# Kernel optimization log

Hardware: AMD Instinct MI355X
Metric: run time of the kernel (lower is better)

Reference implementation:

```python
import jax, jax.numpy as jnp
import numpy as np
import math

S, H, NH, HD = 2048, 1280, 16, 80
WIN = 64
NW = S // WIN
I = 3420
OUT = 3584
L = 8
FULL_IDX = (3, 7)
MERGE = 4  # spatial_merge_size**2
EPS = 1e-6


def setup_inputs() -> dict:
    key = jax.random.key(0)
    ks = jax.random.split(key, 16)
    w = lambda k, s: jax.random.normal(k, s, jnp.float32) * 0.02
    # rotary tables: half-dim freqs duplicated, as in Qwen2.5-VL vision rotary
    inv_freq = 1.0 / (10000.0 ** (np.arange(0, HD // 2, dtype=np.float32) / (HD // 2)))
    freqs = np.outer(np.arange(S, dtype=np.float32), inv_freq)  # [S, HD/2]
    emb = np.concatenate([freqs, freqs], axis=-1)               # [S, HD]
    return {
        "hidden_states": jax.random.normal(ks[0], (S, H), jnp.float32),
        "full_attn_masks": jnp.ones((1, 1, S, S), jnp.float32),
        "window_attn_masks": jnp.ones((NW, 1, WIN, WIN), jnp.float32),
        "cos": jnp.asarray(np.cos(emb)),
        "sin": jnp.asarray(np.sin(emb)),
        "qkv_w": w(ks[1], (L, 3 * H, H)),
        "qkv_b": w(ks[2], (L, 3 * H)),
        "proj_w": w(ks[3], (L, H, H)),
        "proj_b": w(ks[4], (L, H)),
        "norm1_w": jnp.ones((L, H), jnp.float32),
        "norm2_w": jnp.ones((L, H), jnp.float32),
        "gate_w": w(ks[5], (L, I, H)),
        "gate_b": w(ks[6], (L, I)),
        "up_w": w(ks[7], (L, I, H)),
        "up_b": w(ks[8], (L, I)),
        "down_w": w(ks[9], (L, H, I)),
        "down_b": w(ks[10], (L, H)),
        "ln_q_w": jnp.ones((H,), jnp.float32),
        "m0_w": w(ks[11], (H * MERGE, H * MERGE)),
        "m0_b": w(ks[12], (H * MERGE,)),
        "m2_w": w(ks[13], (OUT, H * MERGE)),
        "m2_b": w(ks[14], (OUT,)),
    }


def rmsnorm(x, w):
    v = jnp.mean(jnp.square(x.astype(jnp.float32)), axis=-1, keepdims=True)
    return (x * jax.lax.rsqrt(v + EPS)) * w


def rotate_half(x):
    x1, x2 = jnp.split(x, 2, axis=-1)
    return jnp.concatenate([-x2, x1], axis=-1)


def apply_rope(q, k, cos, sin):
    return q * cos + rotate_half(q) * sin, k * cos + rotate_half(k) * sin


def attn_full(x, mask, cos, sin, qkv_w, qkv_b, proj_w, proj_b):
    # x: [S, H]; mask: [1, 1, S, S] (additive)
    qkv = (x @ qkv_w.T + qkv_b).reshape(S, 3, NH, HD)
    q, k, v = [t[:, i].transpose(1, 0, 2) for i, t in [(0, qkv), (1, qkv), (2, qkv)]]  # [NH, S, HD]
    q, k = apply_rope(q, k, cos, sin)  # cos/sin [S, HD] broadcast over heads
    aw = jnp.einsum('hsd,htd->hst', q, k) / math.sqrt(HD) + mask[0]
    aw = jax.nn.softmax(aw.astype(jnp.float32), axis=-1)
    o = jnp.einsum('hst,htd->hsd', aw, v).transpose(1, 0, 2).reshape(S, NH * HD)
    return o @ proj_w.T + proj_b


def attn_window(x, mask, cos, sin, qkv_w, qkv_b, proj_w, proj_b):
    xw = x.reshape(NW, WIN, H)
    qkv = (xw @ qkv_w.T + qkv_b).reshape(NW, WIN, 3, NH, HD).transpose(2, 0, 3, 1, 4)
    q, k, v = qkv[0], qkv[1], qkv[2]
    cw = cos.reshape(NW, 1, WIN, HD)
    sw = sin.reshape(NW, 1, WIN, HD)
    q, k = apply_rope(q, k, cw, sw)
    aw = jnp.einsum('whsd,whtd->whst', q, k) / math.sqrt(HD) + mask
    aw = jax.nn.softmax(aw.astype(jnp.float32), axis=-1)
    o = jnp.einsum('whst,whtd->whsd', aw, v).transpose(0, 2, 1, 3).reshape(S, NH * HD)
    return o @ proj_w.T + proj_b


def reference(hidden_states, full_attn_masks, window_attn_masks, cos, sin,
              qkv_w, qkv_b, proj_w, proj_b, norm1_w, norm2_w,
              gate_w, gate_b, up_w, up_b, down_w, down_b,
              ln_q_w, m0_w, m0_b, m2_w, m2_b):
    NEG = jnp.finfo(jnp.float32).min
    fm = (1.0 - full_attn_masks) * NEG
    wm = (1.0 - window_attn_masks) * NEG
    x = hidden_states
    for i in range(L):
        h = rmsnorm(x, norm1_w[i])
        if i in FULL_IDX:
            a = attn_full(h, fm, cos, sin, qkv_w[i], qkv_b[i], proj_w[i], proj_b[i])
        else:
            a = attn_window(h, wm, cos, sin, qkv_w[i], qkv_b[i], proj_w[i], proj_b[i])
        x = x + a
        h = rmsnorm(x, norm2_w[i])
        mlp = (jax.nn.silu(h @ gate_w[i].T + gate_b[i]) * (h @ up_w[i].T + up_b[i])) @ down_w[i].T + down_b[i]
        x = x + mlp
    # patch merger: RMSNorm -> merge 4 tokens -> Linear-GELU-Linear
    h = rmsnorm(x, ln_q_w).reshape(-1, H * MERGE)  # [S/4, 5120]
    h = jax.nn.gelu(h @ m0_w.T + m0_b, approximate=False)
    return h @ m2_w.T + m2_b  # [S/4, OUT]
```

## Files before the change

kernel.cpp:

```cpp
#include <hip/hip_runtime.h>
#include <hip/hip_bf16.h>
#include <math.h>

#define S_LEN 2048
#define HID   1280
#define NHEADS 16
#define HDIM  80
#define HDP   96
#define LAYERS 8
#define IDIM  3420
#define IDIMP 3456
#define MERGED 5120
#define OUTD  3584
#define NCH   4
#define CHLEN 512

typedef __attribute__((ext_vector_type(8))) short short8;
typedef __attribute__((ext_vector_type(4))) float f32x4;
typedef unsigned int u32;
typedef __attribute__((address_space(1))) const u32* gptr_t;
typedef __attribute__((address_space(3))) u32* lptr_t;

__device__ inline unsigned short f2b(float f){
  __hip_bfloat16 b = __float2bfloat16(f);
  return __builtin_bit_cast(unsigned short, b);
}
__device__ inline float b2f(unsigned short u){
  return __bfloat162float(__builtin_bit_cast(__hip_bfloat16, u));
}
__device__ inline unsigned pk2(float lo, float hi){
  return (unsigned)f2b(lo) | ((unsigned)f2b(hi) << 16);
}

__global__ __launch_bounds__(256) void convert_kernel(
    const float* __restrict__ src, unsigned short* __restrict__ dst,
    int N, int K, int Np, int Kp)
{
  int kg = Kp >> 3;
  size_t total = (size_t)Np * kg;
  for (size_t i = (size_t)blockIdx.x * 256 + threadIdx.x; i < total;
       i += (size_t)gridDim.x * 256){
    int k8 = (int)(i % kg);
    int n  = (int)(i / kg);
    int k0 = k8 * 8;
    u32 out[4];
    if (n < N && k0 + 8 <= K){
      const float* s = src + (size_t)n * K + k0;
      float4 f0 = *(const float4*)s;
      float4 f1 = *(const float4*)(s + 4);
      out[0] = pk2(f0.x, f0.y); out[1] = pk2(f0.z, f0.w);
      out[2] = pk2(f1.x, f1.y); out[3] = pk2(f1.z, f1.w);
    } else {
      #pragma unroll
      for (int j = 0; j < 4; ++j){
        int ka = k0 + 2 * j;
        float lo = (n < N && ka     < K) ? src[(size_t)n * K + ka]     : 0.f;
        float hi = (n < N && ka + 1 < K) ? src[(size_t)n * K + ka + 1] : 0.f;
        out[j] = pk2(lo, hi);
      }
    }
    *(uint4*)(dst + i * 8) = make_uint4(out[0], out[1], out[2], out[3]);
  }
}

__global__ __launch_bounds__(256) void concat_bias_kernel(
    const float* __restrict__ g, const float* __restrict__ u, float* __restrict__ o)
{
  int n = blockIdx.x * 256 + threadIdx.x;
  if (n >= 2 * IDIMP) return;
  if (n < IDIMP) o[n] = (n < IDIM) ? g[n] : 0.f;
  else { int m2 = n - IDIMP; o[n] = (m2 < IDIM) ? u[m2] : 0.f; }
}

__global__ __launch_bounds__(256) void rmsnorm_kernel(
    const float* __restrict__ x, const float* __restrict__ w,
    unsigned short* __restrict__ out, int H)
{
  int s = blockIdx.x;
  const float* row = x + (size_t)s * H;
  float ss = 0.f;
  for (int c = threadIdx.x; c < H; c += 256){ float v = row[c]; ss += v * v; }
  #pragma unroll
  for (int off = 32; off >= 1; off >>= 1) ss += __shfl_xor(ss, off, 64);
  __shared__ float red[4];
  if ((threadIdx.x & 63) == 0) red[threadIdx.x >> 6] = ss;
  __syncthreads();
  ss = red[0] + red[1] + red[2] + red[3];
  float rs = rsqrtf(ss / H + 1e-6f);
  unsigned short* orow = out + (size_t)s * H;
  for (int c = threadIdx.x; c < H; c += 256) orow[c] = f2b(row[c] * rs * w[c]);
}

template<int EPI, int BM>
__global__ __launch_bounds__(256) void gemm_kernel(
    const unsigned short* __restrict__ A, int lda,
    const unsigned short* __restrict__ B, int ldb,
    const float* __restrict__ bias, int Nact,
    void* __restrict__ Cv, int ldc,
    const float* __restrict__ res,
    int K)
{
  constexpr int MI = BM / 32;
  __shared__ __align__(16) unsigned short As[2][BM * 32];
  __shared__ __align__(16) unsigned short Bs[2][4096];
  const int tid  = threadIdx.x;
  const int lane = tid & 63;
  const int wave = tid >> 6;
  const int wm = wave >> 1, wn = wave & 1;
  const int m0 = blockIdx.y * BM, n0 = blockIdx.x * 128;
  const int l16 = lane & 15, lh = lane >> 4;
  const int lrow = lane >> 2;
  const int lcol = lane & 3;
  f32x4 acc[MI][4] = {};

  auto stage = [&](int bufi, int k0){
    #pragma unroll
    for (int j = 0; j < BM / 64; ++j){
      int chunk = wave * (BM / 64) + j;
      int row  = chunk * 16 + lrow;
      int slot = lcol ^ ((row >> 1) & 3);
      const unsigned short* srcA = A + (size_t)(m0 + row) * lda + k0 + slot * 8;
      __builtin_amdgcn_global_load_lds((gptr_t)srcA, (lptr_t)&As[bufi][chunk * 512], 16, 0, 0);
    }
    #pragma unroll
    for (int j = 0; j < 2; ++j){
      int chunk = wave * 2 + j;
      int row  = chunk * 16 + lrow;
      int slot = lcol ^ ((row >> 1) & 3);
      const unsigned short* srcB = B + (size_t)(n0 + row) * ldb + k0 + slot * 8;
      __builtin_amdgcn_global_load_lds((gptr_t)srcB, (lptr_t)&Bs[bufi][chunk * 512], 16, 0, 0);
    }
  };

  const int nt = K >> 5;
  stage(0, 0);
  __syncthreads();
  int buf = 0;
  for (int t = 0; t < nt; ++t){
    if (t + 1 < nt) stage(buf ^ 1, (t + 1) << 5);
    short8 af[MI], bfr[4];
    #pragma unroll
    for (int mi = 0; mi < MI; ++mi){
      int r = wm * (BM / 2) + mi * 16 + l16;
      int sl = lh ^ ((r >> 1) & 3);
      af[mi] = *(const short8*)&As[buf][r * 32 + sl * 8];
    }
    #pragma unroll
    for (int ni = 0; ni < 4; ++ni){
      int r = wn * 64 + ni * 16 + l16;
      int sl = lh ^ ((r >> 1) & 3);
      bfr[ni] = *(const short8*)&Bs[buf][r * 32 + sl * 8];
    }
    #pragma unroll
    for (int mi = 0; mi < MI; ++mi)
      #pragma unroll
      for (int ni = 0; ni < 4; ++ni)
        acc[mi][ni] = __builtin_amdgcn_mfma_f32_16x16x32_bf16(af[mi], bfr[ni], acc[mi][ni], 0, 0, 0);
    __syncthreads();
    buf ^= 1;
  }

  #pragma unroll
  for (int mi = 0; mi < MI; ++mi){
    int row = m0 + wm * (BM / 2) + mi * 16 + lh * 4;
    #pragma unroll
    for (int ni = 0; ni < 4; ++ni){
      int gn = n0 + wn * 64 + ni * 16 + l16;
      float bv = (gn < Nact) ? bias[gn] : 0.f;
      #pragma unroll
      for (int r2 = 0; r2 < 4; ++r2){
        float v = acc[mi][ni][r2] + bv;
        size_t offc = (size_t)(row + r2) * ldc + gn;
        if (EPI == 0)      ((float*)Cv)[offc] = v;
        else if (EPI == 1) ((float*)Cv)[offc] = res[offc] + v;
        else if (EPI == 2) ((unsigned short*)Cv)[offc] = f2b(0.5f * v * (1.0f + erff(v * 0.70710678118f)));
        else               ((unsigned short*)Cv)[offc] = f2b(v);
      }
    }
  }
}

__global__ __launch_bounds__(256) void rope_split_kernel(
    const unsigned short* __restrict__ qkv, const float* __restrict__ cosT,
    const float* __restrict__ sinT,
    unsigned short* __restrict__ qo, unsigned short* __restrict__ ko,
    unsigned short* __restrict__ vt)
{
  int s = blockIdx.x;
  const unsigned short* row = qkv + (size_t)s * 3840;
  #pragma unroll
  for (int it = 0; it < 5; ++it){
    int idx = it * 256 + threadIdx.x;
    int h = idx / 80, d = idx % 80;
    float qv = b2f(row[h * 80 + d]);
    float kv = b2f(row[1280 + h * 80 + d]);
    float vv = b2f(row[2560 + h * 80 + d]);
    float c  = cosT[s * 80 + d], sn = sinT[s * 80 + d];
    float qr = (d < 40) ? -b2f(row[h * 80 + d + 40])        : b2f(row[h * 80 + d - 40]);
    float kr = (d < 40) ? -b2f(row[1280 + h * 80 + d + 40]) : b2f(row[1280 + h * 80 + d - 40]);
    size_t qkoff = ((size_t)h * S_LEN + s) * HDP + d;
    qo[qkoff] = f2b(qv * c + qr * sn);
    ko[qkoff] = f2b(kv * c + kr * sn);
    vt[((size_t)h * HDIM + d) * S_LEN + s] = f2b(vv);
  }
  int h2 = threadIdx.x >> 4, d2 = 80 + (threadIdx.x & 15);
  size_t poff = ((size_t)h2 * S_LEN + s) * HDP + d2;
  qo[poff] = 0; ko[poff] = 0;
}

template<int PART>
__global__ __launch_bounds__(256) void flash_kernel(
    const unsigned short* __restrict__ q, const unsigned short* __restrict__ k,
    const unsigned short* __restrict__ vt, unsigned short* __restrict__ out,
    float* __restrict__ opart, float* __restrict__ mlpart)
{
  __shared__ __align__(16) unsigned short P[4][16][80];
  const int lane = threadIdx.x & 63;
  const int w = threadIdx.x >> 6;
  const int h = blockIdx.y;
  const int q0 = blockIdx.x * 64;
  const int ch = PART ? blockIdx.z : 0;
  const int qr = q0 + w * 16;
  const int l16 = lane & 15, lh = lane >> 4;
  const unsigned short* qh = q + (size_t)h * S_LEN * HDP;
  const unsigned short* kh = k + (size_t)h * S_LEN * HDP;
  const unsigned short* vh = vt + (size_t)h * HDIM * S_LEN;

  short8 qa[3];
  #pragma unroll
  for (int kc = 0; kc < 3; ++kc)
    qa[kc] = *(const short8*)(qh + (size_t)(qr + l16) * HDP + kc * 32 + lh * 8);

  float m_[4] = {-1e30f, -1e30f, -1e30f, -1e30f};
  float l_[4] = {0.f, 0.f, 0.f, 0.f};
  f32x4 o_[5] = {};
  const int kvb = PART ? ch * CHLEN : q0;
  const int kve = PART ? ch * CHLEN + CHLEN : q0 + 64;

  for (int kv0 = kvb; kv0 < kve; kv0 += 64){
    f32x4 sc[4] = {};
    #pragma unroll
    for (int nf = 0; nf < 4; ++nf){
      const unsigned short* krow = kh + (size_t)(kv0 + nf * 16 + l16) * HDP + lh * 8;
      #pragma unroll
      for (int kc = 0; kc < 3; ++kc){
        short8 bfr = *(const short8*)(krow + kc * 32);
        sc[nf] = __builtin_amdgcn_mfma_f32_16x16x32_bf16(qa[kc], bfr, sc[nf], 0, 0, 0);
      }
    }
    const float scale = 0.11180339887498949f;
    #pragma unroll
    for (int r = 0; r < 4; ++r){
      float t = fmaxf(fmaxf(sc[0][r], sc[1][r]), fmaxf(sc[2][r], sc[3][r])) * scale;
      t = fmaxf(t, __shfl_xor(t, 1, 64));
      t = fmaxf(t, __shfl_xor(t, 2, 64));
      t = fmaxf(t, __shfl_xor(t, 4, 64));
      t = fmaxf(t, __shfl_xor(t, 8, 64));
      float mnew = fmaxf(m_[r], t);
      float corr = __expf(m_[r] - mnew);
      float rs = 0.f;
      #pragma unroll
      for (int nf = 0; nf < 4; ++nf){
        float p = __expf(sc[nf][r] * scale - mnew);
        sc[nf][r] = p;
        rs += p;
      }
      rs += __shfl_xor(rs, 1, 64);
      rs += __shfl_xor(rs, 2, 64);
      rs += __shfl_xor(rs, 4, 64);
      rs += __shfl_xor(rs, 8, 64);
      l_[r] = l_[r] * corr + rs;
      m_[r] = mnew;
      #pragma unroll
      for (int of = 0; of < 5; ++of) o_[of][r] *= corr;
    }
    #pragma unroll
    for (int nf = 0; nf < 4; ++nf)
      #pragma unroll
      for (int r = 0; r < 4; ++r)
        P[w][lh * 4 + r][nf * 16 + l16] = f2b(sc[nf][r]);
    #pragma unroll
    for (int kc2 = 0; kc2 < 2; ++kc2){
      short8 pa = *(const short8*)&P[w][l16][kc2 * 32 + lh * 8];
      #pragma unroll
      for (int of = 0; of < 5; ++of){
        short8 bv = *(const short8*)(vh + (size_t)(of * 16 + l16) * S_LEN + kv0 + kc2 * 32 + lh * 8);
        o_[of] = __builtin_amdgcn_mfma_f32_16x16x32_bf16(pa, bv, o_[of], 0, 0, 0);
      }
    }
  }
  if (PART){
    const size_t base = ((size_t)(ch * NHEADS + h) * S_LEN);
    #pragma unroll
    for (int of = 0; of < 5; ++of)
      #pragma unroll
      for (int r = 0; r < 4; ++r)
        opart[(base + qr + lh * 4 + r) * HDIM + of * 16 + l16] = o_[of][r];
    if (l16 == 0){
      #pragma unroll
      for (int r = 0; r < 4; ++r){
        mlpart[(base + qr + lh * 4 + r) * 2 + 0] = m_[r];
        mlpart[(base + qr + lh * 4 + r) * 2 + 1] = l_[r];
      }
    }
  } else {
    #pragma unroll
    for (int of = 0; of < 5; ++of)
      #pragma unroll
      for (int r = 0; r < 4; ++r){
        size_t off = (size_t)(qr + lh * 4 + r) * HID + h * HDIM + of * 16 + l16;
        out[off] = f2b(o_[of][r] / l_[r]);
      }
  }
}

__global__ __launch_bounds__(256) void flash_reduce_kernel(
    const float* __restrict__ opart, const float* __restrict__ mlpart,
    unsigned short* __restrict__ out)
{
  int idx = blockIdx.x * 256 + threadIdx.x;
  if (idx >= NHEADS * S_LEN * HDIM) return;
  int d = idx % HDIM; int rem = idx / HDIM;
  int qi = rem % S_LEN; int h = rem / S_LEN;
  float mv[NCH];
  float M = -1e30f;
  #pragma unroll
  for (int c = 0; c < NCH; ++c){
    mv[c] = mlpart[((size_t)(c * NHEADS + h) * S_LEN + qi) * 2];
    M = fmaxf(M, mv[c]);
  }
  float L = 0.f, O = 0.f;
  #pragma unroll
  for (int c = 0; c < NCH; ++c){
    float wgt = __expf(mv[c] - M);
    L += wgt * mlpart[((size_t)(c * NHEADS + h) * S_LEN + qi) * 2 + 1];
    O += wgt * opart[((size_t)(c * NHEADS + h) * S_LEN + qi) * HDIM + d];
  }
  out[(size_t)qi * HID + h * HDIM + d] = f2b(O / L);
}

__global__ __launch_bounds__(256) void silu_mul_kernel(
    const float* __restrict__ gu, unsigned short* __restrict__ out)
{
  size_t i = ((size_t)blockIdx.x * 256 + threadIdx.x) * 4;
  if (i >= (size_t)S_LEN * IDIMP) return;
  int row = (int)(i / IDIMP), col = (int)(i % IDIMP);
  float4 gv = *(const float4*)(gu + (size_t)row * (2 * IDIMP) + col);
  float4 uv = *(const float4*)(gu + (size_t)row * (2 * IDIMP) + IDIMP + col);
  float r0 = gv.x / (1.f + __expf(-gv.x)) * uv.x;
  float r1 = gv.y / (1.f + __expf(-gv.y)) * uv.y;
  float r2 = gv.z / (1.f + __expf(-gv.z)) * uv.z;
  float r3 = gv.w / (1.f + __expf(-gv.w)) * uv.w;
  uint2 o;
  o.x = pk2(r0, r1); o.y = pk2(r2, r3);
  *(uint2*)(out + i) = o;
}

static inline int cgrid(size_t total){
  size_t b = (total + 255) / 256;
  return (int)(b < 4096 ? b : 4096);
}

extern "C" void kernel_launch(void* const* d_in, const int* in_sizes, int n_in,
                              void* d_out, int out_size, void* d_ws, size_t ws_size,
                              hipStream_t stream)
{
  const float* hidden = (const float*)d_in[0];
  const float* cosT   = (const float*)d_in[3];
  const float* sinT   = (const float*)d_in[4];
  const float* qkv_w  = (const float*)d_in[5];
  const float* qkv_b  = (const float*)d_in[6];
  const float* proj_w = (const float*)d_in[7];
  const float* proj_b = (const float*)d_in[8];
  const float* norm1_w= (const float*)d_in[9];
  const float* norm2_w= (const float*)d_in[10];
  const float* gate_w = (const float*)d_in[11];
  const float* gate_b = (const float*)d_in[12];
  const float* up_w   = (const float*)d_in[13];
  const float* up_b   = (const float*)d_in[14];
  const float* down_w = (const float*)d_in[15];
  const float* down_b = (const float*)d_in[16];
  const float* ln_q_w = (const float*)d_in[17];
  const float* m0_w   = (const float*)d_in[18];
  const float* m0_b   = (const float*)d_in[19];
  const float* m2_w   = (const float*)d_in[20];
  const float* m2_b   = (const float*)d_in[21];

  char* ws = (char*)d_ws;
  size_t off = 0;
  auto carve = [&](size_t bytes)->char*{
    char* p = ws + off; off += (bytes + 255) & ~(size_t)255; return p;
  };
  float*          x    = (float*)         carve((size_t)S_LEN * HID * 4);
  unsigned short* hbuf = (unsigned short*)carve((size_t)S_LEN * HID * 2);
  unsigned short* qkvb = (unsigned short*)carve((size_t)S_LEN * 3840 * 2);
  unsigned short* qp   = (unsigned short*)carve((size_t)NHEADS * S_LEN * HDP * 2);
  unsigned short* kp   = (unsigned short*)carve((size_t)NHEADS * S_LEN * HDP * 2);
  unsigned short* vtb  = (unsigned short*)carve((size_t)NHEADS * HDIM * S_LEN * 2);
  unsigned short* ao   = (unsigned short*)carve((size_t)S_LEN * HID * 2);
  float*          gbuf = (float*)         carve((size_t)S_LEN * 2 * IDIMP * 4);
  unsigned short* mlp  = (unsigned short*)carve((size_t)S_LEN * IDIMP * 2);
  unsigned short* mg   = (unsigned short*)carve((size_t)512 * MERGED * 2);
  float*          opart= (float*)         carve((size_t)NCH * NHEADS * S_LEN * HDIM * 4);
  float*          mlpt = (float*)         carve((size_t)NCH * NHEADS * S_LEN * 2 * 4);
  float*          cbias= (float*)         carve((size_t)2 * IDIMP * 4);
  unsigned short* wbig = (unsigned short*)carve((size_t)45000000 * 2);
  unsigned short* wqkv = wbig;
  unsigned short* wproj= wbig +  4915200;
  unsigned short* wgate= wproj + 1638400;
  unsigned short* wup  = wgate + (size_t)IDIMP * HID;
  unsigned short* wdown= wup   + (size_t)IDIMP * HID;
  unsigned short* wm0  = wbig;
  unsigned short* wm2  = wbig + (size_t)MERGED * MERGED;
  (void)ws_size; (void)in_sizes; (void)n_in; (void)out_size;

  hipMemcpyAsync(x, hidden, (size_t)S_LEN * HID * 4, hipMemcpyDeviceToDevice, stream);

  for (int i = 0; i < LAYERS; ++i){
    convert_kernel<<<cgrid((size_t)3840*HID/8), 256, 0, stream>>>(
        qkv_w + (size_t)i*3840*HID, wqkv, 3840, HID, 3840, HID);
    convert_kernel<<<cgrid((size_t)HID*HID/8), 256, 0, stream>>>(
        proj_w + (size_t)i*HID*HID, wproj, HID, HID, HID, HID);
    convert_kernel<<<cgrid((size_t)IDIMP*HID/8), 256, 0, stream>>>(
        gate_w + (size_t)i*IDIM*HID, wgate, IDIM, HID, IDIMP, HID);
    convert_kernel<<<cgrid((size_t)IDIMP*HID/8), 256, 0, stream>>>(
        up_w + (size_t)i*IDIM*HID, wup, IDIM, HID, IDIMP, HID);
    convert_kernel<<<cgrid((size_t)HID*IDIMP/8), 256, 0, stream>>>(
        down_w + (size_t)i*HID*IDIM, wdown, HID, IDIM, HID, IDIMP);
    concat_bias_kernel<<<27, 256, 0, stream>>>(
        gate_b + (size_t)i*IDIM, up_b + (size_t)i*IDIM, cbias);

    rmsnorm_kernel<<<S_LEN, 256, 0, stream>>>(x, norm1_w + (size_t)i * HID, hbuf, HID);
    gemm_kernel<3,128><<<dim3(30, 16), 256, 0, stream>>>(
        hbuf, HID, wqkv, HID, qkv_b + (size_t)i * 3840, 3840,
        qkvb, 3840, nullptr, HID);
    rope_split_kernel<<<S_LEN, 256, 0, stream>>>(qkvb, cosT, sinT, qp, kp, vtb);
    if (i == 3 || i == 7){
      flash_kernel<1><<<dim3(32, 16, NCH), 256, 0, stream>>>(qp, kp, vtb, nullptr, opart, mlpt);
      flash_reduce_kernel<<<(NHEADS * S_LEN * HDIM + 255) / 256, 256, 0, stream>>>(opart, mlpt, ao);
    } else {
      flash_kernel<0><<<dim3(32, 16), 256, 0, stream>>>(qp, kp, vtb, ao, nullptr, nullptr);
    }
    gemm_kernel<1,64><<<dim3(10, 32), 256, 0, stream>>>(
        ao, HID, wproj, HID, proj_b + (size_t)i * HID, HID,
        x, HID, x, HID);
    rmsnorm_kernel<<<S_LEN, 256, 0, stream>>>(x, norm2_w + (size_t)i * HID, hbuf, HID);
    gemm_kernel<0,128><<<dim3(54, 16), 256, 0, stream>>>(
        hbuf, HID, wgate, HID, cbias, 2 * IDIMP,
        gbuf, 2 * IDIMP, nullptr, HID);
    silu_mul_kernel<<<(int)(((size_t)S_LEN * IDIMP / 4 + 255) / 256), 256, 0, stream>>>(gbuf, mlp);
    gemm_kernel<1,64><<<dim3(10, 32), 256, 0, stream>>>(
        mlp, IDIMP, wdown, IDIMP, down_b + (size_t)i * HID, HID,
        x, HID, x, IDIMP);
  }
  convert_kernel<<<cgrid((size_t)MERGED*MERGED/8), 256, 0, stream>>>(
      m0_w, wm0, MERGED, MERGED, MERGED, MERGED);
  convert_kernel<<<cgrid((size_t)OUTD*MERGED/8), 256, 0, stream>>>(
      m2_w, wm2, OUTD, MERGED, OUTD, MERGED);
  rmsnorm_kernel<<<S_LEN, 256, 0, stream>>>(x, ln_q_w, hbuf, HID);
  gemm_kernel<2,64><<<dim3(40, 8), 256, 0, stream>>>(
      hbuf, MERGED, wm0, MERGED, m0_b, MERGED, mg, MERGED, nullptr, MERGED);
  gemm_kernel<0,64><<<dim3(28, 8), 256, 0, stream>>>(
      mg, MERGED, wm2, MERGED, m2_b, OUTD, d_out, OUTD, nullptr, MERGED);
}
```

Before: 2.687 ms.

## Rewrite flash attention with 32x32 MFMA, register-resident P, and lazy rescaling

Flash attention now computes S^T with 32x32x16 bf16 MFMA tiles, 32 query rows per wave and 128 per block. The probability tile stays in registers, with a cross-half lane shuffle, instead of round-tripping through LDS. Online-softmax rescaling is skipped unless the running max grows by more than a threshold. The V layout is padded to 96 rows, partial outputs are stored d-major, and the reduce kernel is restructured to normalise per row and stage output through LDS for wider stores. This cuts shuffle reductions, LDS traffic and output write overhead, at the cost of fewer blocks and higher register pressure.

```diff
diff --git a/kernel.cpp b/kernel.cpp
--- a/kernel.cpp
+++ b/kernel.cpp
@@ -7,6 +7,7 @@
 #define NHEADS 16
 #define HDIM  80
 #define HDP   96
+#define VROWS 96
 #define LAYERS 8
 #define IDIM  3420
 #define IDIMP 3456
@@ -17,7 +18,9 @@
 
 typedef __attribute__((ext_vector_type(8))) short short8;
 typedef __attribute__((ext_vector_type(4))) float f32x4;
+typedef __attribute__((ext_vector_type(16))) float f32x16;
 typedef unsigned int u32;
+typedef __attribute__((ext_vector_type(4))) u32 u32x4;
 typedef __attribute__((address_space(1))) const u32* gptr_t;
 typedef __attribute__((address_space(3))) u32* lptr_t;
 
@@ -201,7 +204,7 @@
     size_t qkoff = ((size_t)h * S_LEN + s) * HDP + d;
     qo[qkoff] = f2b(qv * c + qr * sn);
     ko[qkoff] = f2b(kv * c + kr * sn);
-    vt[((size_t)h * HDIM + d) * S_LEN + s] = f2b(vv);
+    vt[((size_t)h * VROWS + d) * S_LEN + s] = f2b(vv);
   }
   int h2 = threadIdx.x >> 4, d2 = 80 + (threadIdx.x & 15);
   size_t poff = ((size_t)h2 * S_LEN + s) * HDP + d2;
@@ -214,103 +217,116 @@
     const unsigned short* __restrict__ vt, unsigned short* __restrict__ out,
     float* __restrict__ opart, float* __restrict__ mlpart)
 {
-  __shared__ __align__(16) unsigned short P[4][16][80];
+  __shared__ unsigned short ot[4][32][88];
   const int lane = threadIdx.x & 63;
   const int w = threadIdx.x >> 6;
   const int h = blockIdx.y;
-  const int q0 = blockIdx.x * 64;
+  const int l31 = lane & 31, lh1 = lane >> 5;
+  const int qr = blockIdx.x * 128 + w * 32;
   const int ch = PART ? blockIdx.z : 0;
-  const int qr = q0 + w * 16;
-  const int l16 = lane & 15, lh = lane >> 4;
   const unsigned short* qh = q + (size_t)h * S_LEN * HDP;
   const unsigned short* kh = k + (size_t)h * S_LEN * HDP;
-  const unsigned short* vh = vt + (size_t)h * HDIM * S_LEN;
-
-  short8 qa[3];
-  #pragma unroll
-  for (int kc = 0; kc < 3; ++kc)
-    qa[kc] = *(const short8*)(qh + (size_t)(qr + l16) * HDP + kc * 32 + lh * 8);
-
-  float m_[4] = {-1e30f, -1e30f, -1e30f, -1e30f};
-  float l_[4] = {0.f, 0.f, 0.f, 0.f};
-  f32x4 o_[5] = {};
-  const int kvb = PART ? ch * CHLEN : q0;
-  const int kve = PART ? ch * CHLEN + CHLEN : q0 + 64;
-
-  for (int kv0 = kvb; kv0 < kve; kv0 += 64){
-    f32x4 sc[4] = {};
-    #pragma unroll
-    for (int nf = 0; nf < 4; ++nf){
-      const unsigned short* krow = kh + (size_t)(kv0 + nf * 16 + l16) * HDP + lh * 8;
+  const unsigned short* vh = vt + (size_t)h * VROWS * S_LEN;
+
+  short8 qa[5];
+  #pragma unroll
+  for (int kc = 0; kc < 5; ++kc)
+    qa[kc] = *(const short8*)(qh + (size_t)(qr + l31) * HDP + kc * 16 + lh1 * 8);
+
+  float m_ = -1e30f, l_ = 0.f;
+  f32x16 o0 = {}, o1 = {}, o2 = {};
+  const int kvb = PART ? ch * CHLEN : (qr & ~63);
+  const int kve = PART ? ch * CHLEN + CHLEN : (qr & ~63) + 64;
+  const float scale = 0.11180339887498949f;
+
+  for (int kvt = kvb; kvt < kve; kvt += 32){
+    f32x16 sc = {};
+    __builtin_amdgcn_s_setprio(1);
+    #pragma unroll
+    for (int kc = 0; kc < 5; ++kc){
+      short8 kf = *(const short8*)(kh + (size_t)(kvt + l31) * HDP + kc * 16 + lh1 * 8);
+      sc = __builtin_amdgcn_mfma_f32_32x32x16_bf16(kf, qa[kc], sc, 0, 0, 0);
+    }
+    __builtin_amdgcn_s_setprio(0);
+    float t = sc[0];
+    #pragma unroll
+    for (int i = 1; i < 16; ++i) t = fmaxf(t, sc[i]);
+    t = fmaxf(t, __shfl_xor(t, 32)) * scale;
+    if (!__all(t <= m_ + 8.f)){
+      float mnew = fmaxf(m_, t);
+      float corr = __expf(m_ - mnew);
+      l_ *= corr;
       #pragma unroll
-      for (int kc = 0; kc < 3; ++kc){
-        short8 bfr = *(const short8*)(krow + kc * 32);
-        sc[nf] = __builtin_amdgcn_mfma_f32_16x16x32_bf16(qa[kc], bfr, sc[nf], 0, 0, 0);
-      }
-    }
-    const float scale = 0.11180339887498949f;
-    #pragma unroll
-    for (int r = 0; r < 4; ++r){
-      float t = fmaxf(fmaxf(sc[0][r], sc[1][r]), fmaxf(sc[2][r], sc[3][r])) * scale;
-      t = fmaxf(t, __shfl_xor(t, 1, 64));
-      t = fmaxf(t, __shfl_xor(t, 2, 64));
-      t = fmaxf(t, __shfl_xor(t, 4, 64));
-      t = fmaxf(t, __shfl_xor(t, 8, 64));
-      float mnew = fmaxf(m_[r], t);
-      float corr = __expf(m_[r] - mnew);
-      float rs = 0.f;
-      #pragma unroll
-      for (int nf = 0; nf < 4; ++nf){
-        float p = __expf(sc[nf][r] * scale - mnew);
-        sc[nf][r] = p;
-        rs += p;
-      }
-      rs += __shfl_xor(rs, 1, 64);
-      rs += __shfl_xor(rs, 2, 64);
-      rs += __shfl_xor(rs, 4, 64);
-      rs += __shfl_xor(rs, 8, 64);
-      l_[r] = l_[r] * corr + rs;
-      m_[r] = mnew;
-      #pragma unroll
-      for (int of = 0; of < 5; ++of) o_[of][r] *= corr;
-    }
-    #pragma unroll
-    for (int nf = 0; nf < 4; ++nf)
-      #pragma unroll
-      for (int r = 0; r < 4; ++r)
-        P[w][lh * 4 + r][nf * 16 + l16] = f2b(sc[nf][r]);
+      for (int i = 0; i < 16; ++i){ o0[i] *= corr; o1[i] *= corr; o2[i] *= corr; }
+      m_ = mnew;
+    }
+    float p[16];
+    float rs = 0.f;
+    #pragma unroll
+    for (int i = 0; i < 16; ++i){ p[i] = __expf(sc[i] * scale - m_); rs += p[i]; }
+    rs += __shfl_xor(rs, 32);
+    l_ += rs;
+    unsigned wd0[4], wd1[4];
+    #pragma unroll
+    for (int j = 0; j < 2; ++j){
+      unsigned Aj = pk2(p[2 * j],     p[2 * j + 1]);
+      unsigned Bj = pk2(p[4 + 2 * j], p[4 + 2 * j + 1]);
+      unsigned t0 = __shfl_xor(Aj, 32);
+      unsigned t1 = __shfl_xor(Bj, 32);
+      wd0[j]     = lh1 ? t1 : Aj;
+      wd0[2 + j] = lh1 ? Bj : t0;
+      Aj = pk2(p[8 + 2 * j],  p[8 + 2 * j + 1]);
+      Bj = pk2(p[12 + 2 * j], p[12 + 2 * j + 1]);
+      t0 = __shfl_xor(Aj, 32);
+      t1 = __shfl_xor(Bj, 32);
+      wd1[j]     = lh1 ? t1 : Aj;
+      wd1[2 + j] = lh1 ? Bj : t0;
+    }
+    __builtin_amdgcn_s_setprio(1);
     #pragma unroll
     for (int kc2 = 0; kc2 < 2; ++kc2){
-      short8 pa = *(const short8*)&P[w][l16][kc2 * 32 + lh * 8];
-      #pragma unroll
-      for (int of = 0; of < 5; ++of){
-        short8 bv = *(const short8*)(vh + (size_t)(of * 16 + l16) * S_LEN + kv0 + kc2 * 32 + lh * 8);
-        o_[of] = __builtin_amdgcn_mfma_f32_16x16x32_bf16(pa, bv, o_[of], 0, 0, 0);
-      }
-    }
-  }
+      u32x4 uw = kc2 ? u32x4{wd1[0], wd1[1], wd1[2], wd1[3]}
+                     : u32x4{wd0[0], wd0[1], wd0[2], wd0[3]};
+      short8 pb = __builtin_bit_cast(short8, uw);
+      const unsigned short* vb = vh + kvt + kc2 * 16 + lh1 * 8;
+      o0 = __builtin_amdgcn_mfma_f32_32x32x16_bf16(
+          *(const short8*)(vb + (size_t)(l31)      * S_LEN), pb, o0, 0, 0, 0);
+      o1 = __builtin_amdgcn_mfma_f32_32x32x16_bf16(
+          *(const short8*)(vb + (size_t)(32 + l31) * S_LEN), pb, o1, 0, 0, 0);
+      o2 = __builtin_amdgcn_mfma_f32_32x32x16_bf16(
+          *(const short8*)(vb + (size_t)(64 + l31) * S_LEN), pb, o2, 0, 0, 0);
+    }
+    __builtin_amdgcn_s_setprio(0);
+  }
+
   if (PART){
-    const size_t base = ((size_t)(ch * NHEADS + h) * S_LEN);
-    #pragma unroll
-    for (int of = 0; of < 5; ++of)
-      #pragma unroll
-      for (int r = 0; r < 4; ++r)
-        opart[(base + qr + lh * 4 + r) * HDIM + of * 16 + l16] = o_[of][r];
-    if (l16 == 0){
-      #pragma unroll
-      for (int r = 0; r < 4; ++r){
-        mlpart[(base + qr + lh * 4 + r) * 2 + 0] = m_[r];
-        mlpart[(base + qr + lh * 4 + r) * 2 + 1] = l_[r];
-      }
+    const size_t hb = (size_t)(ch * NHEADS + h) * 80;
+    #pragma unroll
+    for (int r = 0; r < 16; ++r){
+      int dl = (r & 3) + 8 * (r >> 2) + 4 * lh1;
+      opart[(hb + dl)      * S_LEN + qr + l31] = o0[r];
+      opart[(hb + 32 + dl) * S_LEN + qr + l31] = o1[r];
+      if (dl < 16) opart[(hb + 64 + dl) * S_LEN + qr + l31] = o2[r];
+    }
+    if (lane < 32){
+      size_t mb = ((size_t)(ch * NHEADS + h) * S_LEN + qr + l31) * 2;
+      mlpart[mb] = m_; mlpart[mb + 1] = l_;
     }
   } else {
-    #pragma unroll
-    for (int of = 0; of < 5; ++of)
-      #pragma unroll
-      for (int r = 0; r < 4; ++r){
-        size_t off = (size_t)(qr + lh * 4 + r) * HID + h * HDIM + of * 16 + l16;
-        out[off] = f2b(o_[of][r] / l_[r]);
-      }
+    float inv = 1.f / l_;
+    #pragma unroll
+    for (int r = 0; r < 16; ++r){
+      int dl = (r & 3) + 8 * (r >> 2) + 4 * lh1;
+      ot[w][l31][dl]      = f2b(o0[r] * inv);
+      ot[w][l31][32 + dl] = f2b(o1[r] * inv);
+      if (dl < 16) ot[w][l31][64 + dl] = f2b(o2[r] * inv);
+    }
+    int qq = lane >> 1, half = lane & 1;
+    #pragma unroll
+    for (int j = 0; j < 20; ++j){
+      unsigned v = *(const unsigned*)&ot[w][qq][half * 40 + j * 2];
+      *(unsigned*)&out[(size_t)(qr + qq) * HID + h * HDIM + half * 40 + j * 2] = v;
+    }
   }
 }
 
@@ -318,25 +334,39 @@
     const float* __restrict__ opart, const float* __restrict__ mlpart,
     unsigned short* __restrict__ out)
 {
-  int idx = blockIdx.x * 256 + threadIdx.x;
-  if (idx >= NHEADS * S_LEN * HDIM) return;
-  int d = idx % HDIM; int rem = idx / HDIM;
-  int qi = rem % S_LEN; int h = rem / S_LEN;
-  float mv[NCH];
+  __shared__ float wn[NCH][256];
+  __shared__ unsigned short ot[256][82];
+  const int tid = threadIdx.x;
+  const int h = blockIdx.y;
+  const int q0 = blockIdx.x * 256;
+  float mv[NCH], lv[NCH];
   float M = -1e30f;
   #pragma unroll
   for (int c = 0; c < NCH; ++c){
-    mv[c] = mlpart[((size_t)(c * NHEADS + h) * S_LEN + qi) * 2];
+    size_t mb = ((size_t)(c * NHEADS + h) * S_LEN + q0 + tid) * 2;
+    mv[c] = mlpart[mb]; lv[c] = mlpart[mb + 1];
     M = fmaxf(M, mv[c]);
   }
-  float L = 0.f, O = 0.f;
-  #pragma unroll
-  for (int c = 0; c < NCH; ++c){
-    float wgt = __expf(mv[c] - M);
-    L += wgt * mlpart[((size_t)(c * NHEADS + h) * S_LEN + qi) * 2 + 1];
-    O += wgt * opart[((size_t)(c * NHEADS + h) * S_LEN + qi) * HDIM + d];
-  }
-  out[(size_t)qi * HID + h * HDIM + d] = f2b(O / L);
+  float L = 0.f;
+  #pragma unroll
+  for (int c = 0; c < NCH; ++c){ mv[c] = __expf(mv[c] - M); L += mv[c] * lv[c]; }
+  float invL = 1.f / L;
+  #pragma unroll
+  for (int c = 0; c < NCH; ++c) wn[c][tid] = mv[c] * invL;
+  __syncthreads();
+  for (int d = 0; d < HDIM; ++d){
+    float acc = 0.f;
+    #pragma unroll
+    for (int c = 0; c < NCH; ++c)
+      acc += wn[c][tid] * opart[((size_t)(c * NHEADS + h) * 80 + d) * S_LEN + q0 + tid];
+    ot[tid][d] = f2b(acc);
+  }
+  __syncthreads();
+  #pragma unroll
+  for (int j = 0; j < 40; ++j){
+    unsigned v = *(const unsigned*)&ot[tid][j * 2];
+    *(unsigned*)&out[(size_t)(q0 + tid) * HID + h * HDIM + j * 2] = v;
+  }
 }
 
 __global__ __launch_bounds__(256) void silu_mul_kernel(
@@ -396,12 +426,12 @@
   unsigned short* qkvb = (unsigned short*)carve((size_t)S_LEN * 3840 * 2);
   unsigned short* qp   = (unsigned short*)carve((size_t)NHEADS * S_LEN * HDP * 2);
   unsigned short* kp   = (unsigned short*)carve((size_t)NHEADS * S_LEN * HDP * 2);
-  unsigned short* vtb  = (unsigned short*)carve((size_t)NHEADS * HDIM * S_LEN * 2);
+  unsigned short* vtb  = (unsigned short*)carve((size_t)NHEADS * VROWS * S_LEN * 2);
   unsigned short* ao   = (unsigned short*)carve((size_t)S_LEN * HID * 2);
   float*          gbuf = (float*)         carve((size_t)S_LEN * 2 * IDIMP * 4);
   unsigned short* mlp  = (unsigned short*)carve((size_t)S_LEN * IDIMP * 2);
   unsigned short* mg   = (unsigned short*)carve((size_t)512 * MERGED * 2);
-  float*          opart= (float*)         carve((size_t)NCH * NHEADS * S_LEN * HDIM * 4);
+  float*          opart= (float*)         carve((size_t)NCH * NHEADS * 80 * S_LEN * 4);
   float*          mlpt = (float*)         carve((size_t)NCH * NHEADS * S_LEN * 2 * 4);
   float*          cbias= (float*)         carve((size_t)2 * IDIMP * 4);
   unsigned short* wbig = (unsigned short*)carve((size_t)45000000 * 2);
@@ -436,10 +466,10 @@
         qkvb, 3840, nullptr, HID);
     rope_split_kernel<<<S_LEN, 256, 0, stream>>>(qkvb, cosT, sinT, qp, kp, vtb);
     if (i == 3 || i == 7){
-      flash_kernel<1><<<dim3(32, 16, NCH), 256, 0, stream>>>(qp, kp, vtb, nullptr, opart, mlpt);
-      flash_reduce_kernel<<<(NHEADS * S_LEN * HDIM + 255) / 256, 256, 0, stream>>>(opart, mlpt, ao);
+      flash_kernel<1><<<dim3(16, 16, NCH), 256, 0, stream>>>(qp, kp, vtb, nullptr, opart, mlpt);
+      flash_reduce_kernel<<<dim3(8, 16), 256, 0, stream>>>(opart, mlpt, ao);
     } else {
-      flash_kernel<0><<<dim3(32, 16), 256, 0, stream>>>(qp, kp, vtb, ao, nullptr, nullptr);
+      flash_kernel<0><<<dim3(16, 16), 256, 0, stream>>>(qp, kp, vtb, ao, nullptr, nullptr);
     }
     gemm_kernel<1,64><<<dim3(10, 32), 256, 0, stream>>>(
         ao, HID, wproj, HID, proj_b + (size_t)i * HID, HID,
```

Result: faster. 2.610 ms (-2.9%).
